# Optimization experiments

Measured on AMD Instinct MI355X. Metric: run time of the kernel, lower is better.

Reference implementation:

```python
import jax, jax.numpy as jnp
import numpy as np

L = 2          # lags
D = 64         # latent_size
H = 128        # hidden_dim
NB = 3         # num_layers == n_blocks
B, T = 256, 1024


def setup_inputs() -> dict:
    key = jax.random.key(0)
    ks = jax.random.split(key, 20)
    sd = 0.1
    inp = {
        'x': jax.random.normal(ks[0], (B, T, D), jnp.float32),
        # f1: 3 hidden Linear(L*D=128 -> 128), all same shape so stacked, then out Linear(128 -> 64)
        'f1_hW': jax.random.normal(ks[1], (NB, H, H), jnp.float32) * sd,
        'f1_hb': jax.random.normal(ks[2], (NB, H), jnp.float32) * sd,
        'f1_oW': jax.random.normal(ks[3], (D, H), jnp.float32) * sd,
        'f1_ob': jax.random.normal(ks[4], (D,), jnp.float32) * sd,
        # flow: per block, s_net and t_net each Lin(D,H), Lin(H,H), Lin(H,D) (torch y = x@W.T + b)
        'sW0': jax.random.normal(ks[5], (NB, H, D), jnp.float32) * sd,
        'sb0': jax.random.normal(ks[6], (NB, H), jnp.float32) * sd,
        'sW1': jax.random.normal(ks[7], (NB, H, H), jnp.float32) * sd,
        'sb1': jax.random.normal(ks[8], (NB, H), jnp.float32) * sd,
        'sW2': jax.random.normal(ks[9], (NB, D, H), jnp.float32) * sd,
        'sb2': jax.random.normal(ks[10], (NB, D), jnp.float32) * sd,
        'tW0': jax.random.normal(ks[11], (NB, H, D), jnp.float32) * sd,
        'tb0': jax.random.normal(ks[12], (NB, H), jnp.float32) * sd,
        'tW1': jax.random.normal(ks[13], (NB, H, H), jnp.float32) * sd,
        'tb1': jax.random.normal(ks[14], (NB, H), jnp.float32) * sd,
        'tW2': jax.random.normal(ks[15], (NB, D, H), jnp.float32) * sd,
        'tb2': jax.random.normal(ks[16], (NB, D), jnp.float32) * sd,
    }
    return inp


def _leaky(z):
    return jnp.where(z >= 0, z, 0.2 * z)  # leap's NLayerLeakyMLP uses LeakyReLU(0.2)


def _flow(xt, sW0, sb0, sW1, sb1, sW2, sb2, tW0, tb0, tW1, tb1, tW2, tb2):
    # RealNVP-style affine coupling stack, no batch norm. xt: (N, D)
    m = (jnp.arange(D) % 2).astype(xt.dtype)  # alternating mask, flips per block
    u = xt
    logdet = jnp.zeros((xt.shape[0],), xt.dtype)
    for i in range(NB):
        mx = u * m
        s = jnp.tanh(mx @ sW0[i].T + sb0[i])
        s = jnp.tanh(s @ sW1[i].T + sb1[i])
        s = s @ sW2[i].T + sb2[i]
        t = jax.nn.relu(mx @ tW0[i].T + tb0[i])
        t = jax.nn.relu(t @ tW1[i].T + tb1[i])
        t = t @ tW2[i].T + tb2[i]
        u = mx + (1.0 - m) * (u - t) * jnp.exp(-s)
        logdet = logdet + jnp.sum(-(1.0 - m) * s, axis=1)
        m = 1.0 - m
    return u, logdet


def reference(x, f1_hW, f1_hb, f1_oW, f1_ob, sW0, sb0, sW1, sb1, sW2, sb2,
              tW0, tb0, tW1, tb1, tW2, tb2):
    Bs, Ts, Din = x.shape
    # f2 inverse flow on x[:, L:, :] flattened to (B*(T-L), D)
    xt = x[:, L:, :].reshape(-1, Din)
    x_inv, logdet = _flow(xt, sW0, sb0, sW1, sb1, sW2, sb2,
                          tW0, tb0, tW1, tb1, tW2, tb2)
    x_inv = x_inv.reshape(Bs, Ts - L, Din)
    # vectorized sliding-window MLP (replaces the per-timestep python loop)
    idx = jnp.arange(Ts - L)[:, None] + jnp.arange(L)        # (T-L, L)
    win = x[:, idx, :].reshape(Bs, Ts - L, L * Din)          # (B, T-L, L*D)
    h = win
    for i in range(NB):
        h = _leaky(h @ f1_hW[i].T + f1_hb[i])
    residuals = h @ f1_oW.T + f1_ob - x_inv                  # (B, T-L, D)
    log_abs_det_jacobian = jnp.sum(logdet.reshape(Bs, Ts - L), axis=1)  # (B,)
    return residuals, log_abs_det_jacobian
```

## Files before the change

### kernel.cpp

```cpp
#include <hip/hip_runtime.h>

#define DEV __device__ __forceinline__

typedef __attribute__((ext_vector_type(8)))  short bf16x8;
typedef __attribute__((ext_vector_type(4)))  short s16x4;
typedef __attribute__((ext_vector_type(4)))  float f32x4;
typedef __attribute__((ext_vector_type(16))) float f32x16;
typedef __attribute__((ext_vector_type(4)))  unsigned u32x4;

constexpr int Tt = 1024, TLr = 1022;
constexpr long WSW_BYTES = 704512;

#define MFMA32(a,b,c) __builtin_amdgcn_mfma_f32_32x32x16_bf16((a),(b),(c),0,0,0)

#define GLDS16(gp, lp) __builtin_amdgcn_global_load_lds( \
    (__attribute__((address_space(1))) void*)(void*)(gp), \
    (__attribute__((address_space(3))) void*)(void*)(lp), 16, 0, 0)

#define WAITV4() asm volatile("s_waitcnt vmcnt(4)" ::: "memory")
#define WAITV0() asm volatile("s_waitcnt vmcnt(0)" ::: "memory")
#define BARX()   do { __builtin_amdgcn_s_barrier(); \
                      __builtin_amdgcn_sched_barrier(0); } while(0)

DEV short bf16hi(float f){
  unsigned u = __builtin_bit_cast(unsigned, f);
  u += 0x7FFFu + ((u >> 16) & 1u);
  return (short)(u >> 16);
}
DEV float bf2f(short h){
  unsigned u = ((unsigned)(unsigned short)h) << 16;
  return __builtin_bit_cast(float, u);
}
DEV void splitbf(float f, short &h, short &l){
  h = bf16hi(f);
  l = bf16hi(f - bf2f(h));
}

DEV unsigned cvtpk(float a, float b){
  unsigned r;
  asm("v_cvt_pk_bf16_f32 %0, %1, %2" : "=v"(r) : "v"(a), "v"(b));
  return r;
}
DEV void plswap(unsigned &a, unsigned &b){
  auto r = __builtin_amdgcn_permlane32_swap((int)a, (int)b, false, false);
  a = (unsigned)r[0]; b = (unsigned)r[1];
}

template<int A> DEV float actf(float x){
  if constexpr (A == 1){
    float e = __expf(2.f * x);
    return 1.f - 2.f * __builtin_amdgcn_rcpf(e + 1.f);
  } else if constexpr (A == 2){
    return fmaxf(x, 0.f);
  } else if constexpr (A == 3){
    return x >= 0.f ? x : 0.2f * x;
  }
  return x;
}

DEV void prefStage(const char* __restrict__ wsW, long k, char* dst, int tid){
  const char* s = wsW + (k << 14);
  #pragma unroll
  for (int it = 0; it < 4; ++it)
    GLDS16(s + it * 4096 + tid * 16, dst + it * 4096 + tid * 16);
}

DEV void packTile(const f32x16& c, unsigned (&Bg0)[4], unsigned (&Bg1)[4]){
  unsigned p0 = cvtpk(c[0], c[1]),  p1 = cvtpk(c[2], c[3]);
  unsigned p2 = cvtpk(c[4], c[5]),  p3 = cvtpk(c[6], c[7]);
  plswap(p0, p2); plswap(p1, p3);
  Bg0[0] = p0; Bg0[1] = p1; Bg0[2] = p2; Bg0[3] = p3;
  p0 = cvtpk(c[8],  c[9]);  p1 = cvtpk(c[10], c[11]);
  p2 = cvtpk(c[12], c[13]); p3 = cvtpk(c[14], c[15]);
  plswap(p0, p2); plswap(p1, p3);
  Bg1[0] = p0; Bg1[1] = p1; Bg1[2] = p2; Bg1[3] = p3;
}

template<int KT,int G,int GI,int MOUT,bool LO,int ACT,int MODE>
DEV void computeMT(const char* __restrict__ Ws, const float* __restrict__ bias,
                   const unsigned (&Bin)[2][8][4], unsigned (&Bout)[2][8][4],
                   f32x16 (&uA)[2][2], float (&ldet)[2],
                   float* __restrict__ residBase, int keep, int rowW,
                   int lane, int h4)
{
  constexpr int BS = LO ? 2048 : 1024;
  f32x16 acc[2];
  #pragma unroll
  for (int q = 0; q < 4; ++q){
    f32x4 bv = *(const f32x4*)(bias + 32 * MOUT + 8 * q + h4);
    #pragma unroll
    for (int j = 0; j < 4; ++j){ acc[0][4*q+j] = bv[j]; acc[1][4*q+j] = bv[j]; }
  }
  #pragma unroll
  for (int kt = 0; kt < KT; ++kt){
    const char* wp = Ws + (kt * G + GI) * BS + lane * 16;
    bf16x8 Ah = *(const bf16x8*)wp;
    #pragma unroll
    for (int n = 0; n < 2; ++n){
      u32x4 bw = {Bin[n][kt][0], Bin[n][kt][1], Bin[n][kt][2], Bin[n][kt][3]};
      acc[n] = MFMA32(Ah, __builtin_bit_cast(bf16x8, bw), acc[n]);
    }
    if constexpr (LO){
      bf16x8 Al = *(const bf16x8*)(wp + 1024);
      #pragma unroll
      for (int n = 0; n < 2; ++n){
        u32x4 bw = {Bin[n][kt][0], Bin[n][kt][1], Bin[n][kt][2], Bin[n][kt][3]};
        acc[n] = MFMA32(Al, __builtin_bit_cast(bf16x8, bw), acc[n]);
      }
    }
  }
  if constexpr (MODE == 0){
    #pragma unroll
    for (int n = 0; n < 2; ++n){
      #pragma unroll
      for (int i = 0; i < 16; ++i) acc[n][i] = actf<ACT>(acc[n][i]);
      packTile(acc[n], Bout[n][2 * MOUT], Bout[n][2 * MOUT + 1]);
    }
  } else if constexpr (MODE == 1){
    #pragma unroll
    for (int n = 0; n < 2; ++n)
      #pragma unroll
      for (int r = 0; r < 16; ++r)
        if ((r & 1) != keep) uA[MOUT][n][r] -= acc[n][r];
  } else if constexpr (MODE == 2){
    #pragma unroll
    for (int n = 0; n < 2; ++n)
      #pragma unroll
      for (int r = 0; r < 16; ++r)
        if ((r & 1) != keep){
          uA[MOUT][n][r] *= __expf(-acc[n][r]);
          ldet[n] -= acc[n][r];
        }
  } else {
    const int col = lane & 31;
    #pragma unroll
    for (int n = 0; n < 2; ++n){
      const int tau = rowW + n * 32 + col;
      if (tau < TLr){
        float* rp = residBase + (long)tau * 64 + 32 * MOUT + h4;
        #pragma unroll
        for (int q = 0; q < 4; ++q){
          f32x4 st;
          #pragma unroll
          for (int j = 0; j < 4; ++j)
            st[j] = acc[n][4 * q + j] - uA[MOUT][n][4 * q + j];
          *(f32x4*)(rp + 8 * q) = st;
        }
      }
    }
  }
}

DEV void buildMaskedB(const f32x16 (&u)[2][2], unsigned (&B)[2][8][4], int keep){
  const float mOdd  = (keep == 1) ? 1.f : 0.f;
  const float mEven = 1.f - mOdd;
  #pragma unroll
  for (int n = 0; n < 2; ++n)
    #pragma unroll
    for (int mi = 0; mi < 2; ++mi){
      f32x16 v;
      #pragma unroll
      for (int r = 0; r < 16; ++r)
        v[r] = u[mi][n][r] * ((r & 1) ? mOdd : mEven);
      packTile(v, B[n][2 * mi], B[n][2 * mi + 1]);
    }
}

DEV void buildWin(unsigned (&B)[2][8][4], const float* __restrict__ xb,
                  int rowW, int lane){
  const int col = lane & 31, h = lane >> 5;
  #pragma unroll
  for (int n = 0; n < 2; ++n){
    const int tau = rowW + n * 32 + col;
    #pragma unroll
    for (int g = 0; g < 8; ++g){
      int xr = tau + (g >= 4 ? 1 : 0);
      if (xr > Tt - 1) xr = Tt - 1;
      const int fo = (16 * g + 8 * h) & 63;
      const float* p = xb + xr * 64 + fo;
      f32x4 a = *(const f32x4*)p, b = *(const f32x4*)(p + 4);
      B[n][g][0] = cvtpk(a[0], a[1]); B[n][g][1] = cvtpk(a[2], a[3]);
      B[n][g][2] = cvtpk(b[0], b[1]); B[n][g][3] = cvtpk(b[2], b[3]);
    }
  }
}

__global__ void pnl_conv(const float* __restrict__ sW0, const float* __restrict__ sW1,
                         const float* __restrict__ sW2, const float* __restrict__ tW0,
                         const float* __restrict__ tW1, const float* __restrict__ tW2,
                         const float* __restrict__ f1_hW, const float* __restrict__ f1_oW,
                         char* __restrict__ wsW)
{
  const int cid = blockIdx.x * 256 + threadIdx.x;
  const float* src; long base; int hs, unit, BS, lg; bool LO;
  if (cid < 24576){
    const int blk = cid >> 13, r = cid & 8191;
    const long bb = (long)blk * 196608;
    if      (r < 1024){ src = tW0 + blk*8192;  hs=6; base=bb;        BS=1024; lg=2; LO=false; unit=r; }
    else if (r < 3072){ src = tW1 + blk*16384; hs=7; base=bb+16384;  BS=1024; lg=1; LO=false; unit=r-1024; }
    else if (r < 4096){ src = tW2 + blk*8192;  hs=7; base=bb+49152;  BS=1024; lg=1; LO=false; unit=r-3072; }
    else if (r < 5120){ src = sW0 + blk*8192;  hs=6; base=bb+65536;  BS=2048; lg=1; LO=true;  unit=r-4096; }
    else if (r < 7168){ src = sW1 + blk*16384; hs=7; base=bb+98304;  BS=2048; lg=0; LO=true;  unit=r-5120; }
    else              { src = sW2 + blk*8192;  hs=7; base=bb+163840; BS=2048; lg=0; LO=true;  unit=r-7168; }
  } else {
    const int r = cid - 24576;
    if (r < 6144){ const int l = r >> 11; src = f1_hW + l*16384; hs=7; base=589824+(long)l*32768; BS=1024; lg=1; LO=false; unit=r&2047; }
    else         { src = f1_oW; hs=7; base=688128; BS=1024; lg=1; LO=false; unit=r-6144; }
  }
  const int e    = unit << 3;
  const int feat = e >> hs;
  const int k    = e & ((1 << hs) - 1);
  const int m    = feat >> 5;
  const int stage = m >> lg;
  const int gi    = m & ((1 << lg) - 1);
  const int lane  = (feat & 31) | (((k >> 3) & 1) << 5);
  const long off  = base + (long)stage * 16384
                  + (long)((((k >> 4) << lg) + gi) * BS) + lane * 16;
  const float* sp = src + ((long)feat << hs) + k;
  f32x4 v0 = *(const f32x4*)sp, v1 = *(const f32x4*)(sp + 4);
  s16x4 ha, hb, la, lb;
  #pragma unroll
  for (int j = 0; j < 4; ++j){
    short hh, ll;
    splitbf(v0[j], hh, ll); ha[j] = hh; la[j] = ll;
    splitbf(v1[j], hh, ll); hb[j] = hh; lb[j] = ll;
  }
  *(s16x4*)(wsW + off)     = ha;
  *(s16x4*)(wsW + off + 8) = hb;
  if (LO){
    *(s16x4*)(wsW + off + 1024)     = la;
    *(s16x4*)(wsW + off + 1024 + 8) = lb;
  }
}

#define CMT(KT,G,GI,MOUT,LO,ACT,MODE,WS,BIAS,BIN,BOUT) \
  computeMT<KT,G,GI,MOUT,LO,ACT,MODE>(WS,BIAS,BIN,BOUT,uA,ldet,residBase,keep,rowW,lane,h4)

__global__ __launch_bounds__(256, 2)
void pnl_main(const float* __restrict__ x,
              const float* __restrict__ f1_hb, const float* __restrict__ f1_ob,
              const float* __restrict__ sb0, const float* __restrict__ sb1,
              const float* __restrict__ sb2, const float* __restrict__ tb0,
              const float* __restrict__ tb1, const float* __restrict__ tb2,
              const char* __restrict__ wsW,
              float* __restrict__ resid, float* __restrict__ wsPart)
{
  __shared__ __align__(16) char Wb[49152];
  char* const W0 = Wb;
  char* const W1 = Wb + 16384;
  char* const W2 = Wb + 32768;

  const int tid  = threadIdx.x, w = tid >> 6, lane = tid & 63;
  const int col  = lane & 31, h4 = (lane >> 5) * 4;
  const int bIdx = blockIdx.x >> 2;
  const int t0w  = (blockIdx.x & 3) << 8;
  const int rowW = t0w + w * 64;
  const float* xb = x + (long)bIdx * Tt * 64;
  float* __restrict__ residBase = resid + (long)bIdx * TLr * 64;

  f32x16 uA[2][2];
  #pragma unroll
  for (int mi = 0; mi < 2; ++mi)
    #pragma unroll
    for (int n = 0; n < 2; ++n){
      int xr = rowW + n * 32 + col + 2; if (xr > Tt - 1) xr = Tt - 1;
      #pragma unroll
      for (int q = 0; q < 4; ++q){
        f32x4 v = *(const f32x4*)(xb + xr * 64 + 32 * mi + 8 * q + h4);
        #pragma unroll
        for (int j = 0; j < 4; ++j) uA[mi][n][4 * q + j] = v[j];
      }
    }
  __builtin_amdgcn_sched_barrier(0);

  prefStage(wsW, 0, W0, tid);
  prefStage(wsW, 1, W1, tid);

  float ldet[2] = {0.f, 0.f};
  unsigned Bx[2][8][4], By[2][8][4];

  buildMaskedB(uA, Bx, 1);

  #pragma unroll 1
  for (int blk = 0; blk < 3; ++blk){
    const long kb = (long)blk * 12;
    const int keep = 1 - (blk & 1);
    const float* tb0b = tb0 + blk * 128; const float* tb1b = tb1 + blk * 128;
    const float* tb2b = tb2 + blk * 64;
    const float* sb0b = sb0 + blk * 128; const float* sb1b = sb1 + blk * 128;
    const float* sb2b = sb2 + blk * 64;

    WAITV4(); BARX(); prefStage(wsW, kb + 2, W2, tid);
    CMT(4,4,0,0,false,2,0, W0, tb0b, Bx, By);
    CMT(4,4,1,1,false,2,0, W0, tb0b, Bx, By);
    CMT(4,4,2,2,false,2,0, W0, tb0b, Bx, By);
    CMT(4,4,3,3,false,2,0, W0, tb0b, Bx, By);
    WAITV4(); BARX(); prefStage(wsW, kb + 3, W0, tid);
    CMT(8,2,0,0,false,2,0, W1, tb1b, By, Bx);
    CMT(8,2,1,1,false,2,0, W1, tb1b, By, Bx);
    WAITV4(); BARX(); prefStage(wsW, kb + 4, W1, tid);
    CMT(8,2,0,2,false,2,0, W2, tb1b, By, Bx);
    CMT(8,2,1,3,false,2,0, W2, tb1b, By, Bx);
    WAITV4(); BARX(); prefStage(wsW, kb + 5, W2, tid);
    CMT(8,2,0,0,false,0,1, W0, tb2b, Bx, By);
    CMT(8,2,1,1,false,0,1, W0, tb2b, Bx, By);
    buildMaskedB(uA, By, keep);
    WAITV4(); BARX(); prefStage(wsW, kb + 6, W0, tid);
    CMT(4,2,0,0,true,1,0, W1, sb0b, By, Bx);
    CMT(4,2,1,1,true,1,0, W1, sb0b, By, Bx);
    WAITV4(); BARX(); prefStage(wsW, kb + 7, W1, tid);
    CMT(4,2,0,2,true,1,0, W2, sb0b, By, Bx);
    CMT(4,2,1,3,true,1,0, W2, sb0b, By, Bx);
    WAITV4(); BARX(); prefStage(wsW, kb + 8, W2, tid);
    CMT(8,1,0,0,true,1,0, W0, sb1b, Bx, By);
    WAITV4(); BARX(); prefStage(wsW, kb + 9, W0, tid);
    CMT(8,1,0,1,true,1,0, W1, sb1b, Bx, By);
    WAITV4(); BARX(); prefStage(wsW, kb + 10, W1, tid);
    CMT(8,1,0,2,true,1,0, W2, sb1b, Bx, By);
    WAITV4(); BARX(); prefStage(wsW, kb + 11, W2, tid);
    CMT(8,1,0,3,true,1,0, W0, sb1b, Bx, By);
    WAITV4(); BARX(); prefStage(wsW, kb + 12, W0, tid);
    CMT(8,1,0,0,true,0,2, W1, sb2b, By, Bx);
    WAITV4(); BARX(); prefStage(wsW, kb + 13, W1, tid);
    CMT(8,1,0,1,true,0,2, W2, sb2b, By, Bx);
    if (blk < 2) buildMaskedB(uA, Bx, 1 - ((blk + 1) & 1));
    else         buildWin(Bx, xb, rowW, lane);
  }

  {
    const int keep = 0;
    WAITV4(); BARX(); prefStage(wsW, 38, W2, tid);
    CMT(8,2,0,0,false,3,0, W0, f1_hb, Bx, By);
    CMT(8,2,1,1,false,3,0, W0, f1_hb, Bx, By);
    WAITV4(); BARX(); prefStage(wsW, 39, W0, tid);
    CMT(8,2,0,2,false,3,0, W1, f1_hb, Bx, By);
    CMT(8,2,1,3,false,3,0, W1, f1_hb, Bx, By);
    WAITV4(); BARX(); prefStage(wsW, 40, W1, tid);
    CMT(8,2,0,0,false,3,0, W2, f1_hb + 128, By, Bx);
    CMT(8,2,1,1,false,3,0, W2, f1_hb + 128, By, Bx);
    WAITV4(); BARX(); prefStage(wsW, 41, W2, tid);
    CMT(8,2,0,2,false,3,0, W0, f1_hb + 128, By, Bx);
    CMT(8,2,1,3,false,3,0, W0, f1_hb + 128, By, Bx);
    WAITV4(); BARX(); prefStage(wsW, 42, W0, tid);
    CMT(8,2,0,0,false,3,0, W1, f1_hb + 256, Bx, By);
    CMT(8,2,1,1,false,3,0, W1, f1_hb + 256, Bx, By);
    WAITV4(); BARX();
    CMT(8,2,0,2,false,3,0, W2, f1_hb + 256, Bx, By);
    CMT(8,2,1,3,false,3,0, W2, f1_hb + 256, Bx, By);
    WAITV0(); BARX();
    CMT(8,2,0,0,false,0,3, W0, f1_ob, By, Bx);
    CMT(8,2,1,1,false,0,3, W0, f1_ob, By, Bx);
  }

  const int tau0 = rowW + col, tau1 = rowW + 32 + col;
  float s = (tau0 < TLr ? ldet[0] : 0.f) + (tau1 < TLr ? ldet[1] : 0.f);
  #pragma unroll
  for (int off = 1; off < 64; off <<= 1) s += __shfl_xor(s, off);
  if (lane == 0) wsPart[blockIdx.x * 4 + w] = s;
}

__global__ void pnl_ldet(const float* __restrict__ ws, float* __restrict__ outLd){
  const int b = threadIdx.x;
  float s = 0.f;
  #pragma unroll
  for (int t = 0; t < 16; ++t) s += ws[b * 16 + t];
  outLd[b] = s;
}

extern "C" void kernel_launch(void* const* d_in, const int* in_sizes, int n_in,
                              void* d_out, int out_size, void* d_ws, size_t ws_size,
                              hipStream_t stream){
  const float* x     = (const float*)d_in[0];
  const float* f1_hW = (const float*)d_in[1];
  const float* f1_hb = (const float*)d_in[2];
  const float* f1_oW = (const float*)d_in[3];
  const float* f1_ob = (const float*)d_in[4];
  const float* sW0   = (const float*)d_in[5];
  const float* sb0   = (const float*)d_in[6];
  const float* sW1   = (const float*)d_in[7];
  const float* sb1   = (const float*)d_in[8];
  const float* sW2   = (const float*)d_in[9];
  const float* sb2   = (const float*)d_in[10];
  const float* tW0   = (const float*)d_in[11];
  const float* tb0   = (const float*)d_in[12];
  const float* tW1   = (const float*)d_in[13];
  const float* tb1   = (const float*)d_in[14];
  const float* tW2   = (const float*)d_in[15];
  const float* tb2   = (const float*)d_in[16];

  char*  wsW    = (char*)d_ws;
  float* wsPart = (float*)(wsW + WSW_BYTES);
  float* resid  = (float*)d_out;
  float* outLd  = resid + (long)256 * TLr * 64;

  pnl_conv<<<dim3(124), dim3(256), 0, stream>>>(sW0, sW1, sW2, tW0, tW1, tW2,
                                                f1_hW, f1_oW, wsW);
  pnl_main<<<dim3(1024), dim3(256), 0, stream>>>(
      x, f1_hb, f1_ob, sb0, sb1, sb2, tb0, tb1, tb2, wsW, resid, wsPart);
  pnl_ldet<<<dim3(1), dim3(256), 0, stream>>>(wsPart, outLd);
}
```

Before: 248.3 us.

## Halve per-wave row tile to one 32-row MFMA tile and double grid

Each wave now handles 32 timesteps instead of 64, so the register arrays for activations, accumulators and flow state drop from two N-tiles to one. The grid doubles to 2048 blocks and launch bounds move to 3 blocks per CU to raise occupancy. The trade-off is that each staged weight tile loaded into LDS is reused across half as many MFMAs, and twice as many blocks re-stream the full weight set. The log-det partial reduction is adjusted to 32 partials per batch.

```diff
diff --git a/kernel.cpp b/kernel.cpp
--- a/kernel.cpp
+++ b/kernel.cpp
@@ -78,110 +78,88 @@
 
 template<int KT,int G,int GI,int MOUT,bool LO,int ACT,int MODE>
 DEV void computeMT(const char* __restrict__ Ws, const float* __restrict__ bias,
-                   const unsigned (&Bin)[2][8][4], unsigned (&Bout)[2][8][4],
-                   f32x16 (&uA)[2][2], float (&ldet)[2],
+                   const unsigned (&Bin)[8][4], unsigned (&Bout)[8][4],
+                   f32x16 (&uA)[2], float &ldet,
                    float* __restrict__ residBase, int keep, int rowW,
                    int lane, int h4)
 {
   constexpr int BS = LO ? 2048 : 1024;
-  f32x16 acc[2];
+  f32x16 acc;
   #pragma unroll
   for (int q = 0; q < 4; ++q){
     f32x4 bv = *(const f32x4*)(bias + 32 * MOUT + 8 * q + h4);
     #pragma unroll
-    for (int j = 0; j < 4; ++j){ acc[0][4*q+j] = bv[j]; acc[1][4*q+j] = bv[j]; }
+    for (int j = 0; j < 4; ++j) acc[4 * q + j] = bv[j];
   }
   #pragma unroll
   for (int kt = 0; kt < KT; ++kt){
     const char* wp = Ws + (kt * G + GI) * BS + lane * 16;
     bf16x8 Ah = *(const bf16x8*)wp;
-    #pragma unroll
-    for (int n = 0; n < 2; ++n){
-      u32x4 bw = {Bin[n][kt][0], Bin[n][kt][1], Bin[n][kt][2], Bin[n][kt][3]};
-      acc[n] = MFMA32(Ah, __builtin_bit_cast(bf16x8, bw), acc[n]);
-    }
+    u32x4 bw = {Bin[kt][0], Bin[kt][1], Bin[kt][2], Bin[kt][3]};
+    acc = MFMA32(Ah, __builtin_bit_cast(bf16x8, bw), acc);
     if constexpr (LO){
       bf16x8 Al = *(const bf16x8*)(wp + 1024);
+      acc = MFMA32(Al, __builtin_bit_cast(bf16x8, bw), acc);
+    }
+  }
+  if constexpr (MODE == 0){
+    #pragma unroll
+    for (int i = 0; i < 16; ++i) acc[i] = actf<ACT>(acc[i]);
+    packTile(acc, Bout[2 * MOUT], Bout[2 * MOUT + 1]);
+  } else if constexpr (MODE == 1){
+    #pragma unroll
+    for (int r = 0; r < 16; ++r)
+      if ((r & 1) != keep) uA[MOUT][r] -= acc[r];
+  } else if constexpr (MODE == 2){
+    #pragma unroll
+    for (int r = 0; r < 16; ++r)
+      if ((r & 1) != keep){
+        uA[MOUT][r] *= __expf(-acc[r]);
+        ldet -= acc[r];
+      }
+  } else {
+    const int col = lane & 31;
+    const int tau = rowW + col;
+    if (tau < TLr){
+      float* rp = residBase + (long)tau * 64 + 32 * MOUT + h4;
       #pragma unroll
-      for (int n = 0; n < 2; ++n){
-        u32x4 bw = {Bin[n][kt][0], Bin[n][kt][1], Bin[n][kt][2], Bin[n][kt][3]};
-        acc[n] = MFMA32(Al, __builtin_bit_cast(bf16x8, bw), acc[n]);
+      for (int q = 0; q < 4; ++q){
+        f32x4 st;
+        #pragma unroll
+        for (int j = 0; j < 4; ++j)
+          st[j] = acc[4 * q + j] - uA[MOUT][4 * q + j];
+        *(f32x4*)(rp + 8 * q) = st;
       }
     }
   }
-  if constexpr (MODE == 0){
-    #pragma unroll
-    for (int n = 0; n < 2; ++n){
-      #pragma unroll
-      for (int i = 0; i < 16; ++i) acc[n][i] = actf<ACT>(acc[n][i]);
-      packTile(acc[n], Bout[n][2 * MOUT], Bout[n][2 * MOUT + 1]);
-    }
-  } else if constexpr (MODE == 1){
-    #pragma unroll
-    for (int n = 0; n < 2; ++n)
-      #pragma unroll
-      for (int r = 0; r < 16; ++r)
-        if ((r & 1) != keep) uA[MOUT][n][r] -= acc[n][r];
-  } else if constexpr (MODE == 2){
-    #pragma unroll
-    for (int n = 0; n < 2; ++n)
-      #pragma unroll
-      for (int r = 0; r < 16; ++r)
-        if ((r & 1) != keep){
-          uA[MOUT][n][r] *= __expf(-acc[n][r]);
-          ldet[n] -= acc[n][r];
-        }
-  } else {
-    const int col = lane & 31;
-    #pragma unroll
-    for (int n = 0; n < 2; ++n){
-      const int tau = rowW + n * 32 + col;
-      if (tau < TLr){
-        float* rp = residBase + (long)tau * 64 + 32 * MOUT + h4;
-        #pragma unroll
-        for (int q = 0; q < 4; ++q){
-          f32x4 st;
-          #pragma unroll
-          for (int j = 0; j < 4; ++j)
-            st[j] = acc[n][4 * q + j] - uA[MOUT][n][4 * q + j];
-          *(f32x4*)(rp + 8 * q) = st;
-        }
-      }
-    }
-  }
-}
-
-DEV void buildMaskedB(const f32x16 (&u)[2][2], unsigned (&B)[2][8][4], int keep){
+}
+
+DEV void buildMaskedB(const f32x16 (&u)[2], unsigned (&B)[8][4], int keep){
   const float mOdd  = (keep == 1) ? 1.f : 0.f;
   const float mEven = 1.f - mOdd;
   #pragma unroll
-  for (int n = 0; n < 2; ++n)
-    #pragma unroll
-    for (int mi = 0; mi < 2; ++mi){
-      f32x16 v;
-      #pragma unroll
-      for (int r = 0; r < 16; ++r)
-        v[r] = u[mi][n][r] * ((r & 1) ? mOdd : mEven);
-      packTile(v, B[n][2 * mi], B[n][2 * mi + 1]);
-    }
-}
-
-DEV void buildWin(unsigned (&B)[2][8][4], const float* __restrict__ xb,
+  for (int mi = 0; mi < 2; ++mi){
+    f32x16 v;
+    #pragma unroll
+    for (int r = 0; r < 16; ++r)
+      v[r] = u[mi][r] * ((r & 1) ? mOdd : mEven);
+    packTile(v, B[2 * mi], B[2 * mi + 1]);
+  }
+}
+
+DEV void buildWin(unsigned (&B)[8][4], const float* __restrict__ xb,
                   int rowW, int lane){
   const int col = lane & 31, h = lane >> 5;
-  #pragma unroll
-  for (int n = 0; n < 2; ++n){
-    const int tau = rowW + n * 32 + col;
-    #pragma unroll
-    for (int g = 0; g < 8; ++g){
-      int xr = tau + (g >= 4 ? 1 : 0);
-      if (xr > Tt - 1) xr = Tt - 1;
-      const int fo = (16 * g + 8 * h) & 63;
-      const float* p = xb + xr * 64 + fo;
-      f32x4 a = *(const f32x4*)p, b = *(const f32x4*)(p + 4);
-      B[n][g][0] = cvtpk(a[0], a[1]); B[n][g][1] = cvtpk(a[2], a[3]);
-      B[n][g][2] = cvtpk(b[0], b[1]); B[n][g][3] = cvtpk(b[2], b[3]);
-    }
+  const int tau = rowW + col;
+  #pragma unroll
+  for (int g = 0; g < 8; ++g){
+    int xr = tau + (g >= 4 ? 1 : 0);
+    if (xr > Tt - 1) xr = Tt - 1;
+    const int fo = (16 * g + 8 * h) & 63;
+    const float* p = xb + xr * 64 + fo;
+    f32x4 a = *(const f32x4*)p, b = *(const f32x4*)(p + 4);
+    B[g][0] = cvtpk(a[0], a[1]); B[g][1] = cvtpk(a[2], a[3]);
+    B[g][2] = cvtpk(b[0], b[1]); B[g][3] = cvtpk(b[2], b[3]);
   }
 }
 
@@ -236,7 +214,7 @@
 #define CMT(KT,G,GI,MOUT,LO,ACT,MODE,WS,BIAS,BIN,BOUT) \
   computeMT<KT,G,GI,MOUT,LO,ACT,MODE>(WS,BIAS,BIN,BOUT,uA,ldet,residBase,keep,rowW,lane,h4)
 
-__global__ __launch_bounds__(256, 2)
+__global__ __launch_bounds__(256, 3)
 void pnl_main(const float* __restrict__ x,
               const float* __restrict__ f1_hb, const float* __restrict__ f1_ob,
               const float* __restrict__ sb0, const float* __restrict__ sb1,
@@ -252,32 +230,30 @@
 
   const int tid  = threadIdx.x, w = tid >> 6, lane = tid & 63;
   const int col  = lane & 31, h4 = (lane >> 5) * 4;
-  const int bIdx = blockIdx.x >> 2;
-  const int t0w  = (blockIdx.x & 3) << 8;
-  const int rowW = t0w + w * 64;
+  const int bIdx = blockIdx.x >> 3;
+  const int t0w  = (blockIdx.x & 7) << 7;
+  const int rowW = t0w + w * 32;
   const float* xb = x + (long)bIdx * Tt * 64;
   float* __restrict__ residBase = resid + (long)bIdx * TLr * 64;
 
-  f32x16 uA[2][2];
-  #pragma unroll
-  for (int mi = 0; mi < 2; ++mi)
-    #pragma unroll
-    for (int n = 0; n < 2; ++n){
-      int xr = rowW + n * 32 + col + 2; if (xr > Tt - 1) xr = Tt - 1;
+  f32x16 uA[2];
+  #pragma unroll
+  for (int mi = 0; mi < 2; ++mi){
+    int xr = rowW + col + 2; if (xr > Tt - 1) xr = Tt - 1;
+    #pragma unroll
+    for (int q = 0; q < 4; ++q){
+      f32x4 v = *(const f32x4*)(xb + xr * 64 + 32 * mi + 8 * q + h4);
       #pragma unroll
-      for (int q = 0; q < 4; ++q){
-        f32x4 v = *(const f32x4*)(xb + xr * 64 + 32 * mi + 8 * q + h4);
-        #pragma unroll
-        for (int j = 0; j < 4; ++j) uA[mi][n][4 * q + j] = v[j];
-      }
+      for (int j = 0; j < 4; ++j) uA[mi][4 * q + j] = v[j];
     }
+  }
   __builtin_amdgcn_sched_barrier(0);
 
   prefStage(wsW, 0, W0, tid);
   prefStage(wsW, 1, W1, tid);
 
-  float ldet[2] = {0.f, 0.f};
-  unsigned Bx[2][8][4], By[2][8][4];
+  float ldet = 0.f;
+  unsigned Bx[8][4], By[8][4];
 
   buildMaskedB(uA, Bx, 1);
 
@@ -352,8 +328,8 @@
     CMT(8,2,1,1,false,0,3, W0, f1_ob, By, Bx);
   }
 
-  const int tau0 = rowW + col, tau1 = rowW + 32 + col;
-  float s = (tau0 < TLr ? ldet[0] : 0.f) + (tau1 < TLr ? ldet[1] : 0.f);
+  const int tau = rowW + col;
+  float s = (tau < TLr) ? ldet : 0.f;
   #pragma unroll
   for (int off = 1; off < 64; off <<= 1) s += __shfl_xor(s, off);
   if (lane == 0) wsPart[blockIdx.x * 4 + w] = s;
@@ -363,7 +339,7 @@
   const int b = threadIdx.x;
   float s = 0.f;
   #pragma unroll
-  for (int t = 0; t < 16; ++t) s += ws[b * 16 + t];
+  for (int t = 0; t < 32; ++t) s += ws[b * 32 + t];
   outLd[b] = s;
 }
 
@@ -395,7 +371,7 @@
 
   pnl_conv<<<dim3(124), dim3(256), 0, stream>>>(sW0, sW1, sW2, tW0, tW1, tW2,
                                                 f1_hW, f1_oW, wsW);
-  pnl_main<<<dim3(1024), dim3(256), 0, stream>>>(
+  pnl_main<<<dim3(2048), dim3(256), 0, stream>>>(
       x, f1_hb, f1_ob, sb0, sb1, sb2, tb0, tb1, tb2, wsW, resid, wsPart);
   pnl_ldet<<<dim3(1), dim3(256), 0, stream>>>(wsPart, outLd);
 }
```

New measurement: 262.0 us. +5.5%, slower.
